# Performance work log

Hardware: AMD Instinct MI355X
Metric: run time of the kernel (lower is better)

The kernel has to match this reference:

```python
import jax, jax.numpy as jnp
import numpy as np

N_HEADS = 16
N_KV_HEADS = 4
WINDOW = 128
THETA = 10000.0


def _rope_cos_sin(T, half):
    inv = 1.0 / (THETA ** (jnp.arange(half, dtype=jnp.float32) / half))
    f = jnp.arange(T, dtype=jnp.float32)[:, None] * inv[None, :]  # (T, half)
    return jnp.cos(f), jnp.sin(f)


def _apply_rope(x, cos, sin):
    # x: (B, H, T, hd); interleaved (real, imag) pairs like torch view_as_complex
    xr, xi = x[..., 0::2], x[..., 1::2]
    out_r = xr * cos - xi * sin
    out_i = xr * sin + xi * cos
    return jnp.stack([out_r, out_i], axis=-1).reshape(x.shape)


def setup_inputs() -> dict:
    key = jax.random.key(0)
    ks = jax.random.split(key, 6)
    B, T, C = 1, 4096, 2048
    kvC = (C // N_HEADS) * N_KV_HEADS
    return {
        "x": jax.random.normal(ks[0], (B, T, C), dtype=jnp.float32),
        "wq": jax.random.normal(ks[1], (C, C), dtype=jnp.float32) * 0.02,
        "wk": jax.random.normal(ks[2], (C, kvC), dtype=jnp.float32) * 0.02,
        "wv": jax.random.normal(ks[3], (C, kvC), dtype=jnp.float32) * 0.02,
        "wo": jax.random.normal(ks[4], (C, C), dtype=jnp.float32) * 0.02,
        "sink": jnp.zeros((1, N_HEADS, 1, 1), dtype=jnp.float32),
    }


def reference(x, wq, wk, wv, wo, sink):
    B, T, C = x.shape
    hd = C // N_HEADS
    n_rep = N_HEADS // N_KV_HEADS

    q = (x @ wq).reshape(B, T, N_HEADS, hd).transpose(0, 2, 1, 3)    # (B,H,T,hd)
    k = (x @ wk).reshape(B, T, N_KV_HEADS, hd).transpose(0, 2, 1, 3)  # (B,Hkv,T,hd)
    v = (x @ wv).reshape(B, T, N_KV_HEADS, hd).transpose(0, 2, 1, 3)

    cos, sin = _rope_cos_sin(T, hd // 2)  # (T, hd/2), broadcasts over (B,H,T,hd/2)
    q = _apply_rope(q, cos, sin)
    k = _apply_rope(k, cos, sin)

    # GQA head expansion (repeat_interleave over head dim)
    k = jnp.repeat(k, n_rep, axis=1)
    v = jnp.repeat(v, n_rep, axis=1)

    att = jnp.einsum("bhqd,bhkd->bhqk", q, k) * (hd ** -0.5) + sink

    # symmetric sliding-window band: |i - j| <= window//2
    idx = jnp.arange(T)
    band = jnp.abs(idx[:, None] - idx[None, :]) <= (WINDOW // 2)
    att = jnp.where(band[None, None, :, :], att, -jnp.inf)

    att = jax.nn.softmax(att, axis=-1)
    # torch code replaces NaN rows (fully-masked) with uniform; band always has diag so no-op
    att = jnp.where(jnp.isnan(att), 1.0 / T, att)

    out = jnp.einsum("bhqk,bhkd->bqhd", att, v).reshape(B, T, C)
    return out @ wo
```

## Files before the change

kernel.cpp:

```cpp
#include <hip/hip_runtime.h>
#include <stdint.h>

#define T_SEQ 4096
#define C_DIM 2048
#define HD 128

typedef unsigned short ushort_t;
typedef __attribute__((ext_vector_type(8))) short shortx8;
typedef __attribute__((ext_vector_type(4))) float floatx4;
typedef __attribute__((ext_vector_type(8))) unsigned short u16x8;
typedef __attribute__((ext_vector_type(4))) unsigned short u16x4;

__device__ __forceinline__ ushort_t f2bf(float f) {
  union { float f; uint32_t u; } v; v.f = f;
  v.u += 0x7fffu + ((v.u >> 16) & 1u);
  return (ushort_t)(v.u >> 16);
}
__device__ __forceinline__ void load_lds16(const ushort_t* g, ushort_t* l) {
  __builtin_amdgcn_global_load_lds(
      (const __attribute__((address_space(1))) unsigned int*)g,
      (__attribute__((address_space(3))) unsigned int*)l, 16, 0, 0);
}

__global__ __launch_bounds__(256) void prep_kernel(
    const float* __restrict__ wq, const float* __restrict__ wk,
    const float* __restrict__ wv, const float* __restrict__ wo,
    const float* __restrict__ x,
    ushort_t* __restrict__ BtAll, ushort_t* __restrict__ woT,
    ushort_t* __restrict__ xb) {
  const int bid = blockIdx.x;
  const int tid = threadIdx.x;
  if (bid >= 2560) {
    int i = (bid - 2560) * 256 + tid;
    float4 v = ((const float4*)x)[i];
    u16x4 o; o[0] = f2bf(v.x); o[1] = f2bf(v.y); o[2] = f2bf(v.z); o[3] = f2bf(v.w);
    ((u16x4*)xb)[i] = o;
    return;
  }
  const float* src; ushort_t* dst; int C, bx, by;
  if (bid < 1024) { src = wq; dst = BtAll; C = 2048; bx = bid & 31; by = bid >> 5; }
  else if (bid < 1280) { int b = bid - 1024; src = wk; dst = BtAll + (size_t)2048 * 2048; C = 512; bx = b & 7; by = b >> 3; }
  else if (bid < 1536) { int b = bid - 1280; src = wv; dst = BtAll + (size_t)2560 * 2048; C = 512; bx = b & 7; by = b >> 3; }
  else { int b = bid - 1536; src = wo; dst = woT; C = 2048; bx = b & 31; by = b >> 5; }
  const int R = 2048;

  __shared__ float tile[64][65];
  const int c0 = bx * 64, r0 = by * 64;
  for (int i = tid; i < 1024; i += 256) {
    int r = i >> 4, cc = (i & 15) * 4;
    float4 v = *(const float4*)&src[(size_t)(r0 + r) * C + c0 + cc];
    tile[r][cc] = v.x; tile[r][cc + 1] = v.y; tile[r][cc + 2] = v.z; tile[r][cc + 3] = v.w;
  }
  __syncthreads();
  for (int i = tid; i < 512; i += 256) {
    int oc = i >> 3;
    int g = (i & 7) * 8;
    u16x8 o;
    for (int j = 0; j < 8; ++j) o[j] = f2bf(tile[g + j][oc]);
    *(u16x8*)&dst[(size_t)(c0 + oc) * R + r0 + g] = o;
  }
}

struct GemmAcc { floatx4 a[4][4]; };

__device__ __forceinline__ void gemm_core_bk64(
    const ushort_t* __restrict__ A, const ushort_t* __restrict__ Bt,
    ushort_t* As, ushort_t* Bs, GemmAcc& acc,
    int m0, int n0, int K, int tid, int lane, int wave, int quad, int l16,
    int wm, int wn) {
  const int nk = K >> 6;
  for (int kk = 0; kk < nk; ++kk) {
    const int k0 = kk << 6;
    for (int r = 0; r < 4; ++r) {
      int e = r * 256 + tid;
      int row = e >> 3;
      int p = e & 7;
      int g = (p - row) & 7;
      const ushort_t* ga = A + (size_t)(m0 + row) * K + k0 + g * 8;
      const ushort_t* gb = Bt + (size_t)(n0 + row) * K + k0 + g * 8;
      ushort_t* la = As + (size_t)(r * 256 + (tid & 192)) * 8;
      ushort_t* lb = Bs + (size_t)(r * 256 + (tid & 192)) * 8;
      load_lds16(ga, la);
      load_lds16(gb, lb);
    }
    __syncthreads();
    for (int ks = 0; ks < 2; ++ks) {
      shortx8 af[4], bfr[4];
      for (int i = 0; i < 4; ++i) {
        int ar = wm + i * 16 + l16;
        af[i] = *(const shortx8*)(As + ar * 64 + (((ks << 2) + quad + ar) & 7) * 8);
        int br = wn + i * 16 + l16;
        bfr[i] = *(const shortx8*)(Bs + br * 64 + (((ks << 2) + quad + br) & 7) * 8);
      }
      for (int i = 0; i < 4; ++i)
        for (int j = 0; j < 4; ++j)
          acc.a[i][j] = __builtin_amdgcn_mfma_f32_16x16x32_bf16(af[i], bfr[j], acc.a[i][j], 0, 0, 0);
    }
    __syncthreads();
  }
}

__global__ __launch_bounds__(256, 3) void gemm_qkv(
    const ushort_t* __restrict__ A, const ushort_t* __restrict__ Bt,
    ushort_t* __restrict__ qbb, ushort_t* __restrict__ kbb,
    ushort_t* __restrict__ vtb) {
  __shared__ __align__(16) ushort_t As[128 * 64];
  __shared__ __align__(16) ushort_t Bs[128 * 64];
  const int tid = threadIdx.x;
  const int lane = tid & 63;
  const int wave = tid >> 6;
  const int quad = lane >> 4;
  const int l16 = lane & 15;
  const int m0 = blockIdx.y * 128;
  const int n0 = blockIdx.x * 128;
  const int wm = (wave & 1) * 64;
  const int wn = (wave >> 1) * 64;

  GemmAcc acc = {};
  gemm_core_bk64(A, Bt, As, Bs, acc, m0, n0, 2048, tid, lane, wave, quad, l16, wm, wn);

  if (blockIdx.x < 20) {
    const bool isq = (blockIdx.x < 16);
    const int par = l16 & 1;
    for (int j = 0; j < 4; ++j) {
      int col = n0 + wn + j * 16 + l16;
      int irot = (col & 127) >> 1;
      float inv = __expf(-0.14391157f * (float)irot);
      for (int i = 0; i < 4; ++i) {
        int t0r = m0 + wm + i * 16 + quad * 4;
        for (int r = 0; r < 4; ++r) {
          float val = acc.a[i][j][r];
          float other = __shfl_xor(val, 1, 64);
          float sn, cs;
          __sincosf((float)(t0r + r) * inv, &sn, &cs);
          float outv = par ? (other * sn + val * cs) : (val * cs - other * sn);
          if (isq) qbb[(size_t)(t0r + r) * 2048 + col] = f2bf(outv);
          else     kbb[(size_t)(t0r + r) * 512 + (col - 2048)] = f2bf(outv);
        }
      }
    }
  } else {
    for (int j = 0; j < 4; ++j) {
      int dim = n0 + wn + j * 16 + l16 - 2560;
      for (int i = 0; i < 4; ++i) {
        int t0r = m0 + wm + i * 16 + quad * 4;
        u16x4 o;
        for (int r = 0; r < 4; ++r) o[r] = f2bf(acc.a[i][j][r]);
        *(u16x4*)&vtb[(size_t)dim * T_SEQ + t0r] = o;
      }
    }
  }
}

__global__ __launch_bounds__(256, 3) void gemm_bf16(
    const ushort_t* __restrict__ A, const ushort_t* __restrict__ Bt,
    float* __restrict__ C, int M, int N, int K) {
  __shared__ __align__(16) ushort_t As[128 * 64];
  __shared__ __align__(16) ushort_t Bs[128 * 64];
  const int tid = threadIdx.x;
  const int lane = tid & 63;
  const int wave = tid >> 6;
  const int quad = lane >> 4;
  const int l16 = lane & 15;
  const int m0 = blockIdx.y * 128;
  const int n0 = blockIdx.x * 128;
  const int wm = (wave & 1) * 64;
  const int wn = (wave >> 1) * 64;

  GemmAcc acc = {};
  gemm_core_bk64(A, Bt, As, Bs, acc, m0, n0, K, tid, lane, wave, quad, l16, wm, wn);

  for (int i = 0; i < 4; ++i)
    for (int j = 0; j < 4; ++j) {
      int col = n0 + wn + j * 16 + l16;
      int rbase = m0 + wm + i * 16 + quad * 4;
      for (int r = 0; r < 4; ++r)
        C[(size_t)(rbase + r) * N + col] = acc.a[i][j][r];
    }
}

#define LSTR 168
__global__ __launch_bounds__(512, 1) void attn_kernel(
    const ushort_t* __restrict__ qbb, const ushort_t* __restrict__ kbb,
    const ushort_t* __restrict__ vtb, ushort_t* __restrict__ ao) {
  __shared__ __align__(16) ushort_t QP[128 * LSTR];
  __shared__ __align__(16) ushort_t KV[160 * LSTR];

  const int tid = threadIdx.x;
  const int lane = tid & 63;
  const int wave = tid >> 6;
  const int l16 = lane & 15;
  const int quad = lane >> 4;
  const int kvh = blockIdx.x;
  const int h0 = kvh * 4;
  const int t0 = blockIdx.y * 32;
  const int kstart = t0 - 64;
  const int hsel = wave & 3;
  const int qh = wave >> 2;
  const float scale = 0.08838834764831845f;

  for (int c = tid; c < 2048; c += 512) {
    int row = c >> 4, c8 = c & 15;
    int h = h0 + (row >> 5);
    int q = t0 + (row & 31);
    u16x8 v = *(const u16x8*)&qbb[(size_t)q * C_DIM + h * HD + c8 * 8];
    *(u16x8*)&QP[row * LSTR + c8 * 8] = v;
  }
  for (int c = tid; c < 2560; c += 512) {
    int row = c >> 4, c8 = c & 15;
    int t = kstart + row;
    u16x8 v;
    if (t >= 0 && t < T_SEQ) {
      v = *(const u16x8*)&kbb[(size_t)t * 512 + kvh * HD + c8 * 8];
    } else {
      for (int z = 0; z < 8; ++z) v[z] = 0;
    }
    *(u16x8*)&KV[row * LSTR + c8 * 8] = v;
  }
  __syncthreads();

  floatx4 acc[10] = {};
  const int arow = hsel * 32 + qh * 16 + l16;
  for (int ks = 0; ks < 4; ++ks) {
    shortx8 af = *(const shortx8*)&QP[arow * LSTR + ks * 32 + quad * 8];
    for (int kt = 0; kt < 10; ++kt) {
      shortx8 bf = *(const shortx8*)&KV[(kt * 16 + l16) * LSTR + ks * 32 + quad * 8];
      acc[kt] = __builtin_amdgcn_mfma_f32_16x16x32_bf16(af, bf, acc[kt], 0, 0, 0);
    }
  }

  float mrow[4] = {-3e38f, -3e38f, -3e38f, -3e38f};
  for (int kt = 0; kt < 10; ++kt) {
    int col = kt * 16 + l16;
    int kg = kstart + col;
    for (int r = 0; r < 4; ++r) {
      int row = qh * 16 + quad * 4 + r;
      bool valid = (kg >= 0) && (kg < T_SEQ) && (col >= row) && (col <= row + 128);
      float s = valid ? acc[kt][r] * scale : -3e38f;
      acc[kt][r] = s;
      mrow[r] = fmaxf(mrow[r], s);
    }
  }
  for (int off = 1; off < 16; off <<= 1)
    for (int r = 0; r < 4; ++r)
      mrow[r] = fmaxf(mrow[r], __shfl_xor(mrow[r], off, 64));
  float rl[4];
  for (int r = 0; r < 4; ++r) {
    float s = 0.f;
    for (int kt = 0; kt < 10; ++kt) {
      float p = __expf(acc[kt][r] - mrow[r]);
      acc[kt][r] = p;
      s += p;
    }
    rl[r] = s;
  }
  for (int off = 1; off < 16; off <<= 1)
    for (int r = 0; r < 4; ++r) rl[r] += __shfl_xor(rl[r], off, 64);
  for (int r = 0; r < 4; ++r) rl[r] = 1.0f / rl[r];

  __syncthreads();

  for (int kt = 0; kt < 10; ++kt) {
    int col = kt * 16 + l16;
    for (int r = 0; r < 4; ++r) {
      int row = hsel * 32 + qh * 16 + quad * 4 + r;
      QP[row * LSTR + col] = f2bf(acc[kt][r] * rl[r]);
    }
  }
  for (int c = tid; c < 2560; c += 512) {
    int dim = c / 20, c8 = c % 20;
    int k0 = kstart + c8 * 8;
    const ushort_t* g = &vtb[(size_t)(kvh * HD + dim) * T_SEQ];
    u16x8 v;
    if (k0 >= 0 && k0 + 7 < T_SEQ) {
      v = *(const u16x8*)&g[k0];
    } else {
      for (int z = 0; z < 8; ++z) {
        int kk = k0 + z;
        v[z] = (kk >= 0 && kk < T_SEQ) ? g[kk] : (ushort_t)0;
      }
    }
    *(u16x8*)&KV[dim * LSTR + c8 * 8] = v;
  }
  __syncthreads();

  floatx4 oacc[8] = {};
  const int prow = hsel * 32 + qh * 16 + l16;
  for (int ks = 0; ks < 5; ++ks) {
    shortx8 pf = *(const shortx8*)&QP[prow * LSTR + ks * 32 + quad * 8];
    for (int dt = 0; dt < 8; ++dt) {
      shortx8 vf = *(const shortx8*)&KV[(dt * 16 + l16) * LSTR + ks * 32 + quad * 8];
      oacc[dt] = __builtin_amdgcn_mfma_f32_16x16x32_bf16(pf, vf, oacc[dt], 0, 0, 0);
    }
  }

  const int h = h0 + hsel;
  for (int r = 0; r < 4; ++r) {
    int row = t0 + qh * 16 + quad * 4 + r;
    for (int dt = 0; dt < 8; ++dt) {
      int dim = dt * 16 + l16;
      ao[(size_t)row * C_DIM + h * HD + dim] = f2bf(oacc[dt][r]);
    }
  }
}

extern "C" void kernel_launch(void* const* d_in, const int* in_sizes, int n_in,
                              void* d_out, int out_size, void* d_ws, size_t ws_size,
                              hipStream_t stream) {
  const float* x  = (const float*)d_in[0];
  const float* wq = (const float*)d_in[1];
  const float* wk = (const float*)d_in[2];
  const float* wv = (const float*)d_in[3];
  const float* wo = (const float*)d_in[4];
  float* out = (float*)d_out;

  char* ws = (char*)d_ws;
  ushort_t* BtAll = (ushort_t*)(ws);
  ushort_t* woT   = (ushort_t*)(ws + 12582912);
  ushort_t* xb    = (ushort_t*)(ws + 20971520);
  ushort_t* qbb   = (ushort_t*)(ws + 37748736);
  ushort_t* kbb   = (ushort_t*)(ws + 54525952);
  ushort_t* vtb   = (ushort_t*)(ws + 58720256);
  ushort_t* ao    = (ushort_t*)(ws + 62914560);

  prep_kernel<<<10752, 256, 0, stream>>>(wq, wk, wv, wo, x, BtAll, woT, xb);

  gemm_qkv<<<dim3(24, 32), 256, 0, stream>>>(xb, BtAll, qbb, kbb, vtb);

  attn_kernel<<<dim3(4, 128), 512, 0, stream>>>(qbb, kbb, vtb, ao);

  gemm_bf16<<<dim3(16, 32), 256, 0, stream>>>(ao, woT, out, 4096, 2048, 2048);
}
```

Baseline: 234.9 us.

## Double query rows per attention block to reuse K/V window tiles

```diff
diff --git a/kernel.cpp b/kernel.cpp
--- a/kernel.cpp
+++ b/kernel.cpp
@@ -179,12 +179,14 @@
     }
 }
 
-#define LSTR 168
+#define QSTR 168
+#define KSTR 168
+#define VSTR 216
 __global__ __launch_bounds__(512, 1) void attn_kernel(
     const ushort_t* __restrict__ qbb, const ushort_t* __restrict__ kbb,
     const ushort_t* __restrict__ vtb, ushort_t* __restrict__ ao) {
-  __shared__ __align__(16) ushort_t QP[128 * LSTR];
-  __shared__ __align__(16) ushort_t KV[160 * LSTR];
+  __shared__ __align__(16) ushort_t QP[256 * QSTR];
+  __shared__ __align__(16) ushort_t KV[208 * KSTR];
 
   const int tid = threadIdx.x;
   const int lane = tid & 63;
@@ -193,20 +195,20 @@
   const int quad = lane >> 4;
   const int kvh = blockIdx.x;
   const int h0 = kvh * 4;
-  const int t0 = blockIdx.y * 32;
+  const int t0 = blockIdx.y * 64;
   const int kstart = t0 - 64;
   const int hsel = wave & 3;
   const int qh = wave >> 2;
   const float scale = 0.08838834764831845f;
 
-  for (int c = tid; c < 2048; c += 512) {
+  for (int c = tid; c < 4096; c += 512) {
     int row = c >> 4, c8 = c & 15;
-    int h = h0 + (row >> 5);
-    int q = t0 + (row & 31);
+    int h = h0 + (row >> 6);
+    int q = t0 + (row & 63);
     u16x8 v = *(const u16x8*)&qbb[(size_t)q * C_DIM + h * HD + c8 * 8];
-    *(u16x8*)&QP[row * LSTR + c8 * 8] = v;
-  }
-  for (int c = tid; c < 2560; c += 512) {
+    *(u16x8*)&QP[row * QSTR + c8 * 8] = v;
+  }
+  for (int c = tid; c < 3328; c += 512) {
     int row = c >> 4, c8 = c & 15;
     int t = kstart + row;
     u16x8 v;
@@ -215,60 +217,77 @@
     } else {
       for (int z = 0; z < 8; ++z) v[z] = 0;
     }
-    *(u16x8*)&KV[row * LSTR + c8 * 8] = v;
+    *(u16x8*)&KV[row * KSTR + c8 * 8] = v;
   }
   __syncthreads();
 
-  floatx4 acc[10] = {};
-  const int arow = hsel * 32 + qh * 16 + l16;
+  const int qb0 = qh * 32, qb1 = qb0 + 16;
+  const int tb0 = qb0 >> 4, tb1 = tb0 + 1;
+  floatx4 acc0[10] = {}, acc1[10] = {};
   for (int ks = 0; ks < 4; ++ks) {
-    shortx8 af = *(const shortx8*)&QP[arow * LSTR + ks * 32 + quad * 8];
+    shortx8 af0 = *(const shortx8*)&QP[(hsel * 64 + qb0 + l16) * QSTR + ks * 32 + quad * 8];
+    shortx8 af1 = *(const shortx8*)&QP[(hsel * 64 + qb1 + l16) * QSTR + ks * 32 + quad * 8];
     for (int kt = 0; kt < 10; ++kt) {
-      shortx8 bf = *(const shortx8*)&KV[(kt * 16 + l16) * LSTR + ks * 32 + quad * 8];
-      acc[kt] = __builtin_amdgcn_mfma_f32_16x16x32_bf16(af, bf, acc[kt], 0, 0, 0);
-    }
-  }
-
-  float mrow[4] = {-3e38f, -3e38f, -3e38f, -3e38f};
-  for (int kt = 0; kt < 10; ++kt) {
-    int col = kt * 16 + l16;
-    int kg = kstart + col;
+      shortx8 bf0 = *(const shortx8*)&KV[((tb0 + kt) * 16 + l16) * KSTR + ks * 32 + quad * 8];
+      acc0[kt] = __builtin_amdgcn_mfma_f32_16x16x32_bf16(af0, bf0, acc0[kt], 0, 0, 0);
+      shortx8 bf1 = *(const shortx8*)&KV[((tb1 + kt) * 16 + l16) * KSTR + ks * 32 + quad * 8];
+      acc1[kt] = __builtin_amdgcn_mfma_f32_16x16x32_bf16(af1, bf1, acc1[kt], 0, 0, 0);
+    }
+  }
+
+  float rl0[4], rl1[4];
+#pragma unroll
+  for (int s = 0; s < 2; ++s) {
+    floatx4* acc = s ? acc1 : acc0;
+    const int qb = s ? qb1 : qb0;
+    const int tb = s ? tb1 : tb0;
+    float* rl = s ? rl1 : rl0;
+    float mrow[4] = {-3e38f, -3e38f, -3e38f, -3e38f};
+    for (int kt = 0; kt < 10; ++kt) {
+      int col = (tb + kt) * 16 + l16;
+      int kg = kstart + col;
+      for (int r = 0; r < 4; ++r) {
+        int qrow = qb + quad * 4 + r;
+        bool valid = (kg >= 0) && (kg < T_SEQ) && (col >= qrow) && (col <= qrow + 128);
+        float sc = valid ? acc[kt][r] * scale : -3e38f;
+        acc[kt][r] = sc;
+        mrow[r] = fmaxf(mrow[r], sc);
+      }
+    }
+    for (int off = 1; off < 16; off <<= 1)
+      for (int r = 0; r < 4; ++r)
+        mrow[r] = fmaxf(mrow[r], __shfl_xor(mrow[r], off, 64));
     for (int r = 0; r < 4; ++r) {
-      int row = qh * 16 + quad * 4 + r;
-      bool valid = (kg >= 0) && (kg < T_SEQ) && (col >= row) && (col <= row + 128);
-      float s = valid ? acc[kt][r] * scale : -3e38f;
-      acc[kt][r] = s;
-      mrow[r] = fmaxf(mrow[r], s);
-    }
-  }
-  for (int off = 1; off < 16; off <<= 1)
-    for (int r = 0; r < 4; ++r)
-      mrow[r] = fmaxf(mrow[r], __shfl_xor(mrow[r], off, 64));
-  float rl[4];
-  for (int r = 0; r < 4; ++r) {
-    float s = 0.f;
+      float ss = 0.f;
+      for (int kt = 0; kt < 10; ++kt) {
+        float p = __expf(acc[kt][r] - mrow[r]);
+        acc[kt][r] = p;
+        ss += p;
+      }
+      rl[r] = ss;
+    }
+    for (int off = 1; off < 16; off <<= 1)
+      for (int r = 0; r < 4; ++r) rl[r] += __shfl_xor(rl[r], off, 64);
+    for (int r = 0; r < 4; ++r) rl[r] = 1.0f / rl[r];
+  }
+
+  __syncthreads();
+
+#pragma unroll
+  for (int s = 0; s < 2; ++s) {
+    floatx4* acc = s ? acc1 : acc0;
+    const int qb = s ? qb1 : qb0;
+    float* rl = s ? rl1 : rl0;
     for (int kt = 0; kt < 10; ++kt) {
-      float p = __expf(acc[kt][r] - mrow[r]);
-      acc[kt][r] = p;
-      s += p;
-    }
-    rl[r] = s;
-  }
-  for (int off = 1; off < 16; off <<= 1)
-    for (int r = 0; r < 4; ++r) rl[r] += __shfl_xor(rl[r], off, 64);
-  for (int r = 0; r < 4; ++r) rl[r] = 1.0f / rl[r];
-
-  __syncthreads();
-
-  for (int kt = 0; kt < 10; ++kt) {
-    int col = kt * 16 + l16;
-    for (int r = 0; r < 4; ++r) {
-      int row = hsel * 32 + qh * 16 + quad * 4 + r;
-      QP[row * LSTR + col] = f2bf(acc[kt][r] * rl[r]);
-    }
-  }
-  for (int c = tid; c < 2560; c += 512) {
-    int dim = c / 20, c8 = c % 20;
+      int col = kt * 16 + l16;
+      for (int r = 0; r < 4; ++r) {
+        int row = hsel * 64 + qb + quad * 4 + r;
+        QP[row * QSTR + col] = f2bf(acc[kt][r] * rl[r]);
+      }
+    }
+  }
+  for (int c = tid; c < 3328; c += 512) {
+    int dim = c / 26, c8 = c % 26;
     int k0 = kstart + c8 * 8;
     const ushort_t* g = &vtb[(size_t)(kvh * HD + dim) * T_SEQ];
     u16x8 v;
@@ -280,26 +299,29 @@
         v[z] = (kk >= 0 && kk < T_SEQ) ? g[kk] : (ushort_t)0;
       }
     }
-    *(u16x8*)&KV[dim * LSTR + c8 * 8] = v;
+    *(u16x8*)&KV[dim * VSTR + c8 * 8] = v;
   }
   __syncthreads();
 
-  floatx4 oacc[8] = {};
-  const int prow = hsel * 32 + qh * 16 + l16;
-  for (int ks = 0; ks < 5; ++ks) {
-    shortx8 pf = *(const shortx8*)&QP[prow * LSTR + ks * 32 + quad * 8];
-    for (int dt = 0; dt < 8; ++dt) {
-      shortx8 vf = *(const shortx8*)&KV[(dt * 16 + l16) * LSTR + ks * 32 + quad * 8];
-      oacc[dt] = __builtin_amdgcn_mfma_f32_16x16x32_bf16(pf, vf, oacc[dt], 0, 0, 0);
-    }
-  }
-
-  const int h = h0 + hsel;
-  for (int r = 0; r < 4; ++r) {
-    int row = t0 + qh * 16 + quad * 4 + r;
-    for (int dt = 0; dt < 8; ++dt) {
-      int dim = dt * 16 + l16;
-      ao[(size_t)row * C_DIM + h * HD + dim] = f2bf(oacc[dt][r]);
+#pragma unroll
+  for (int s = 0; s < 2; ++s) {
+    const int qb = s ? qb1 : qb0;
+    const int prow = hsel * 64 + qb + l16;
+    floatx4 oacc[8] = {};
+    for (int ks = 0; ks < 5; ++ks) {
+      shortx8 pf = *(const shortx8*)&QP[prow * QSTR + ks * 32 + quad * 8];
+      for (int dt = 0; dt < 8; ++dt) {
+        shortx8 vf = *(const shortx8*)&KV[(dt * 16 + l16) * VSTR + qb + ks * 32 + quad * 8];
+        oacc[dt] = __builtin_amdgcn_mfma_f32_16x16x32_bf16(pf, vf, oacc[dt], 0, 0, 0);
+      }
+    }
+    const int h = h0 + hsel;
+    for (int r = 0; r < 4; ++r) {
+      int row = t0 + qb + quad * 4 + r;
+      for (int dt = 0; dt < 8; ++dt) {
+        int dim = dt * 16 + l16;
+        ao[(size_t)row * C_DIM + h * HD + dim] = f2bf(oacc[dt][r]);
+      }
     }
   }
 }
@@ -327,7 +349,7 @@
 
   gemm_qkv<<<dim3(24, 32), 256, 0, stream>>>(xb, BtAll, qbb, kbb, vtb);
 
-  attn_kernel<<<dim3(4, 128), 512, 0, stream>>>(qbb, kbb, vtb, ao);
+  attn_kernel<<<dim3(4, 64), 512, 0, stream>>>(qbb, kbb, vtb, ao);
 
   gemm_bf16<<<dim3(16, 32), 256, 0, stream>>>(ao, woT, out, 4096, 2048, 2048);
 }
```

Result: no change. 236.1 us (+0.5%).
